# Performance work log

Measured on AMD Instinct MI355X. Metric: run time of the kernel, lower is better.

Reference implementation:

```python
import jax, jax.numpy as jnp
import numpy as np

B, S = 32, 128
VIDEO_SIZE, TITLE_SIZE = 768, 768
NUM_TAG, NUM_VOCAB, HIDDEN = 10000, 21128, 256


def setup_inputs() -> dict:
    key = jax.random.key(0)
    ks = jax.random.split(key, 10)
    video_feature = jax.random.normal(ks[0], (B, VIDEO_SIZE), dtype=jnp.float32)
    title_feature = jax.random.normal(ks[1], (B, S, TITLE_SIZE), dtype=jnp.float32)
    label_tag = jax.random.uniform(ks[2], (B, NUM_TAG), dtype=jnp.float32)
    label_mlm = jax.random.randint(ks[3], (B, S), 0, NUM_VOCAB, dtype=jnp.int64)
    Wt = jax.random.normal(ks[4], (NUM_TAG, VIDEO_SIZE), dtype=jnp.float32) * 0.02
    bt = jnp.zeros((NUM_TAG,), dtype=jnp.float32)
    Wm = jax.random.normal(ks[5], (NUM_VOCAB, TITLE_SIZE), dtype=jnp.float32) * 0.02
    bm = jnp.zeros((NUM_VOCAB,), dtype=jnp.float32)
    Wh = jax.random.normal(ks[6], (HIDDEN, VIDEO_SIZE + TITLE_SIZE), dtype=jnp.float32) * 0.02
    bh = jnp.zeros((HIDDEN,), dtype=jnp.float32)
    return {
        "video_feature": video_feature,
        "title_feature": title_feature,
        "label_tag": label_tag,
        "label_mlm": label_mlm,
        "Wt": Wt, "bt": bt, "Wm": Wm, "bm": bm, "Wh": Wh, "bh": bh,
    }


def reference(video_feature, title_feature, label_tag, label_mlm, Wt, bt, Wm, bm, Wh, bh):
    # tag head + BCEWithLogits (mean reduction), numerically stable form
    pred_tag = video_feature @ Wt.T + bt                       # [B, NUM_TAG]
    loss_tag = jnp.mean(
        jnp.maximum(pred_tag, 0.0) - pred_tag * label_tag
        + jnp.log1p(jnp.exp(-jnp.abs(pred_tag)))
    )
    pred_tag_sig = jax.nn.sigmoid(pred_tag)

    # mlm head: per-token vocab logits, masked CE summed over nonzero labels
    logits = jnp.einsum('bsd,vd->bsv', title_feature, Wm) + bm  # [B, S, V]
    lse = jax.nn.logsumexp(logits, axis=-1)                     # [B, S]
    gold = jnp.take_along_axis(logits, label_mlm[..., None], axis=-1)[..., 0]
    ce = lse - gold                                             # per-token NLL
    mask = (label_mlm != 0)
    loss_mlm = jnp.sum(jnp.where(mask, ce, 0.0))

    # fused embedding head + L2 normalize (torch eps 1e-12)
    feature = jnp.concatenate([video_feature, title_feature[:, 0]], axis=1)
    embedding = feature @ Wh.T + bh                             # [B, HIDDEN]
    norm = jnp.linalg.norm(embedding, axis=1, keepdims=True)
    normed_embedding = embedding / jnp.maximum(norm, 1e-12)

    return (pred_tag_sig, normed_embedding, loss_tag, loss_mlm)
```

## Files before the change

### kernel.cpp

```cpp
#include <hip/hip_runtime.h>
#include <hip/hip_bf16.h>
#include <math.h>

typedef short bf16x8 __attribute__((ext_vector_type(8)));
typedef float f32x4 __attribute__((ext_vector_type(4)));
typedef long i64x2 __attribute__((ext_vector_type(2)));

#define KDIM 768
#define NTAG 10000
#define NVOC 21128
#define HID 256
#define NTOK 4096
#define NCHUNK 24
#define CHUNK 881
#define NTILE 56
#define M0 4.0f
#define WMSCALE 16.0f
#define INVSCALE 0.0625f
#define LOG2E 1.44269504f

#define WS_A     0ull
#define WS_AVID  3145728ull
#define WS_PSUM  3194880ull
#define WS_GOLD  3588096ull
#define WS_TAGL  3604480ull
#define WS_WM8   3604544ull
#define WS_NEED  (WS_WM8 + 16226304ull + 65536ull)

#define OUT_EMB  320000
#define OUT_LTAG 328192
#define OUT_LMLM 328193

#define TAG_BLKS 313
#define GOLD_BLKS 1024
#define EMB_BLKS 32

typedef const __attribute__((address_space(1))) unsigned int glds_g;
typedef __attribute__((address_space(3))) unsigned int glds_l;

static __device__ __forceinline__ unsigned short f2bf(float f) {
  unsigned u = __builtin_bit_cast(unsigned, f);
  u = u + 0x7FFFu + ((u >> 16) & 1u);
  return (unsigned short)(u >> 16);
}

static __device__ __forceinline__ int pk4_fp8(float4 v, float scale) {
  int w = __builtin_amdgcn_cvt_pk_fp8_f32(v.x * scale, v.y * scale, 0, false);
  w = __builtin_amdgcn_cvt_pk_fp8_f32(v.z * scale, v.w * scale, w, true);
  return w;
}

__global__ __launch_bounds__(256) void k_conv(
    const float* __restrict__ title, const float* __restrict__ video,
    const float* __restrict__ Wm,
    char* __restrict__ A8, unsigned short* __restrict__ Avid,
    char* __restrict__ Wm8, float* __restrict__ tagSum) {
  const int nT = 393216;
  const int nV = 3072;
  const int nW = 2028288;
  int i = blockIdx.x * 256 + threadIdx.x;
  if (i == 0) tagSum[0] = 0.f;
  if (i < nT) {
    float4 v0 = ((const float4*)title)[i * 2];
    float4 v1 = ((const float4*)title)[i * 2 + 1];
    int2 o = {pk4_fp8(v0, 1.f), pk4_fp8(v1, 1.f)};
    *(int2*)(A8 + (size_t)i * 8) = o;
  } else if (i < nT + nV) {
    int j = i - nT;
    float4 v0 = ((const float4*)video)[j * 2];
    float4 v1 = ((const float4*)video)[j * 2 + 1];
    bf16x8 o;
    o[0] = (short)f2bf(v0.x); o[1] = (short)f2bf(v0.y);
    o[2] = (short)f2bf(v0.z); o[3] = (short)f2bf(v0.w);
    o[4] = (short)f2bf(v1.x); o[5] = (short)f2bf(v1.y);
    o[6] = (short)f2bf(v1.z); o[7] = (short)f2bf(v1.w);
    *(bf16x8*)(Avid + (size_t)j * 8) = o;
  } else {
    int j = i - nT - nV;
    if (j >= nW) return;
    float4 v0 = ((const float4*)Wm)[j * 2];
    float4 v1 = ((const float4*)Wm)[j * 2 + 1];
    int2 o = {pk4_fp8(v0, WMSCALE), pk4_fp8(v1, WMSCALE)};
    int row = j / 96;
    int koff = (j % 96) * 8;
    int kk2 = koff >> 6, w = koff & 63;
    int h = w >> 5, gg = (w & 31) >> 3;
    *(int2*)(Wm8 + (size_t)row * KDIM + kk2 * 64 + gg * 16 + h * 8) = o;
  }
}

template<bool WM8>
__global__ __launch_bounds__(256)
__attribute__((amdgpu_waves_per_eu(3, 3)))
void k_mlm(
    const char* __restrict__ A8,
    const float* __restrict__ Wm,
    const char* __restrict__ Wm8,
    const float* __restrict__ bm,
    float* __restrict__ psum) {
  __shared__ __align__(1024) char Bsm[4][12288];
  __shared__ float biasS[NTILE * 16];
  const int tid = threadIdx.x;
  const int lane = tid & 63, g = lane >> 4, col = lane & 15;
  const int wave = tid >> 6;
  const int chunk = blockIdx.x % NCHUNK, mt = blockIdx.x / NCHUNK;
  const int nbeg = chunk * CHUNK;
  const int nend = min(nbeg + CHUNK, NVOC);

  for (int i = tid; i < NTILE * 16; i += 256) {
    int n = nbeg + i;
    biasS[i] = (n < nend) ? (bm[n] - M0) * LOG2E : -1e30f;
  }

  const int arow0 = mt * 128 + wave * 32;
  long a0[24], a1[24];
  #pragma unroll
  for (int kk = 0; kk < 24; ++kk) {
    a0[kk] = *(const long*)(A8 + (size_t)(arow0 + col) * KDIM + kk * 32 + g * 8);
    a1[kk] = *(const long*)(A8 + (size_t)(arow0 + 16 + col) * KDIM + kk * 32 + g * 8);
  }

  float s[8];
  #pragma unroll
  for (int i = 0; i < 8; ++i) s[i] = 0.f;

  int e[3];
  #pragma unroll
  for (int j = 0; j < 3; ++j) {
    int sg = j * 256 + tid;
    e[j] = (sg & 15) * KDIM + (sg >> 6) * 64 + ((sg >> 4) & 3) * 16;
  }

  const int off0 = col * 16 + g * 256;
  const float kinv = INVSCALE * LOG2E;

  auto COMPUTE = [&](int t) {
    const char* B = &Bsm[t & 3][0] + off0;
    f32x4 acc0 = {0.f, 0.f, 0.f, 0.f}, acc1 = {0.f, 0.f, 0.f, 0.f};
    #pragma unroll
    for (int kk2 = 0; kk2 < 12; ++kk2) {
      i64x2 b = *(const i64x2*)(B + kk2 * 1024);
      acc0 = __builtin_amdgcn_mfma_f32_16x16x32_fp8_fp8(a0[2 * kk2], b[0], acc0, 0, 0, 0);
      acc1 = __builtin_amdgcn_mfma_f32_16x16x32_fp8_fp8(a1[2 * kk2], b[0], acc1, 0, 0, 0);
      acc0 = __builtin_amdgcn_mfma_f32_16x16x32_fp8_fp8(a0[2 * kk2 + 1], b[1], acc0, 0, 0, 0);
      acc1 = __builtin_amdgcn_mfma_f32_16x16x32_fp8_fp8(a1[2 * kk2 + 1], b[1], acc1, 0, 0, 0);
    }
    const float bias2 = biasS[t * 16 + col];
    #pragma unroll
    for (int rr = 0; rr < 4; ++rr) {
      s[rr]     += exp2f(fmaf(acc0[rr], kinv, bias2));
      s[rr + 4] += exp2f(fmaf(acc1[rr], kinv, bias2));
    }
  };

  if constexpr (WM8) {
    auto STAGE = [&](int buf, int tt) {
      const char* src = Wm8 + (size_t)(nbeg + tt * 16) * KDIM;
      char* dst = &Bsm[buf][0] + wave * 1024;
      #pragma unroll
      for (int j = 0; j < 3; ++j) {
        __builtin_amdgcn_global_load_lds((glds_g*)(src + e[j]),
                                         (glds_l*)(dst + j * 4096), 16, 0, 0);
      }
    };
    STAGE(0, 0); STAGE(1, 1); STAGE(2, 2);
    asm volatile("s_waitcnt lgkmcnt(0)" ::: "memory");
    for (int t = 0; t < NTILE; ++t) {
      asm volatile("s_waitcnt vmcnt(6)" ::: "memory");
      __builtin_amdgcn_s_barrier();
      __builtin_amdgcn_sched_barrier(0);
      int tp = t + 3;
      STAGE((t + 3) & 3, (tp < NTILE) ? tp : 0);
      __builtin_amdgcn_s_setprio(1);
      COMPUTE(t);
      __builtin_amdgcn_s_setprio(0);
      __builtin_amdgcn_sched_barrier(0);
    }
  } else {
    __syncthreads();
    for (int t = 0; t < NTILE; ++t) {
      #pragma unroll
      for (int j = 0; j < 3; ++j) {
        int sg = j * 256 + tid;
        int n = nbeg + t * 16 + (sg & 15);
        int kk2 = sg >> 6, gg = (sg >> 4) & 3;
        int4 o = {0, 0, 0, 0};
        if (n < NVOC) {
          const float* wp = Wm + (size_t)n * KDIM + kk2 * 64 + gg * 8;
          float4 f0 = ((const float4*)wp)[0], f1 = ((const float4*)wp)[1];
          float4 f2 = ((const float4*)(wp + 32))[0], f3 = ((const float4*)(wp + 32))[1];
          o.x = pk4_fp8(f0, WMSCALE); o.y = pk4_fp8(f1, WMSCALE);
          o.z = pk4_fp8(f2, WMSCALE); o.w = pk4_fp8(f3, WMSCALE);
        }
        *(int4*)(&Bsm[0][0] + sg * 16) = o;
      }
      __syncthreads();
      COMPUTE(t);
      __syncthreads();
    }
  }

  #pragma unroll
  for (int i = 0; i < 8; ++i) {
    float v = s[i];
    v += __shfl_xor(v, 1);
    v += __shfl_xor(v, 2);
    v += __shfl_xor(v, 4);
    v += __shfl_xor(v, 8);
    s[i] = v;
  }
  if (col == 0) {
    #pragma unroll
    for (int mblk = 0; mblk < 2; ++mblk)
      #pragma unroll
      for (int rr = 0; rr < 4; ++rr) {
        int tok = arow0 + mblk * 16 + g * 4 + rr;
        psum[tok * NCHUNK + chunk] = s[mblk * 4 + rr];
      }
  }
}

__global__ __launch_bounds__(256) void k_tail(
    const unsigned short* __restrict__ Avid,
    const float* __restrict__ Wt, const float* __restrict__ bt,
    const float* __restrict__ ylab,
    const float* __restrict__ title, const int* __restrict__ lab,
    const float* __restrict__ Wm, const float* __restrict__ bm,
    const float* __restrict__ video,
    const float* __restrict__ Wh, const float* __restrict__ bh,
    float* __restrict__ out_sig, float* __restrict__ tagSum,
    float* __restrict__ gold, float* __restrict__ out_emb) {
  __shared__ __align__(1024) char smem[49664];
  const int bid = blockIdx.x, tid = threadIdx.x;
  const int wave = tid >> 6, lane = tid & 63, g = lane >> 4, col = lane & 15;

  if (bid < TAG_BLKS) {
    unsigned short* Bt = (unsigned short*)smem;
    float* wsum = (float*)(smem + 49152);
    #pragma unroll
    for (int j = 0; j < 12; ++j) {
      int sg = j * 256 + tid;
      int tt = (j >= 6) ? 1 : 0;
      int sgl = sg - tt * 1536;
      int kk = sgl >> 6, c = (sgl & 63) >> 2, gg = sgl & 3;
      int n = (bid * 2 + tt) * 16 + c;
      bf16x8 o = {};
      if (n < NTAG) {
        const float* wp = Wt + (size_t)n * KDIM + kk * 32 + gg * 8;
        float4 f0 = ((const float4*)wp)[0], f1 = ((const float4*)wp)[1];
        o[0] = (short)f2bf(f0.x); o[1] = (short)f2bf(f0.y);
        o[2] = (short)f2bf(f0.z); o[3] = (short)f2bf(f0.w);
        o[4] = (short)f2bf(f1.x); o[5] = (short)f2bf(f1.y);
        o[6] = (short)f2bf(f1.z); o[7] = (short)f2bf(f1.w);
      }
      *(bf16x8*)((char*)Bt + sg * 16) = o;
    }
    __syncthreads();

    const int ntile = bid * 2 + (wave >> 1), mhalf = wave & 1;
    float lacc = 0.f;
    if (ntile < 625) {
      bf16x8 a[24];
      #pragma unroll
      for (int kk = 0; kk < 24; ++kk)
        a[kk] = *(const bf16x8*)(Avid + (size_t)(mhalf * 16 + col) * KDIM + kk * 32 + g * 8);
      const char* Bb = (const char*)Bt + (wave >> 1) * 24576 + col * 64 + g * 16;
      f32x4 acc = {0.f, 0.f, 0.f, 0.f};
      #pragma unroll
      for (int kk = 0; kk < 24; ++kk) {
        bf16x8 b = *(const bf16x8*)(Bb + kk * 1024);
        acc = __builtin_amdgcn_mfma_f32_16x16x32_bf16(a[kk], b, acc, 0, 0, 0);
      }
      const int nc = ntile * 16 + col;
      if (nc < NTAG) {
        const float bias = bt[nc];
        #pragma unroll
        for (int rr = 0; rr < 4; ++rr) {
          int brow = mhalf * 16 + g * 4 + rr;
          float x = acc[rr] + bias;
          out_sig[(size_t)brow * NTAG + nc] = 1.f / (1.f + __expf(-x));
          float y = ylab[(size_t)brow * NTAG + nc];
          lacc += fmaxf(x, 0.f) - x * y + log1pf(__expf(-fabsf(x)));
        }
      }
    }
    #pragma unroll
    for (int m = 32; m; m >>= 1) lacc += __shfl_xor(lacc, m);
    if (lane == 0) wsum[wave] = lacc;
    __syncthreads();
    if (tid == 0) atomicAdd(tagSum, wsum[0] + wsum[1] + wsum[2] + wsum[3]);

  } else if (bid < TAG_BLKS + GOLD_BLKS) {
    int tok = (bid - TAG_BLKS) * 4 + wave;
    int l = lab[tok];
    float acc = 0.f;
    #pragma unroll
    for (int j = 0; j < 12; ++j) {
      int k = j * 64 + lane;
      acc += title[(size_t)tok * KDIM + k] * Wm[(size_t)l * KDIM + k];
    }
    #pragma unroll
    for (int m = 32; m; m >>= 1) acc += __shfl_xor(acc, m);
    if (lane == 0) gold[tok] = acc + bm[l];

  } else {
    float* feat = (float*)smem;
    float* red = (float*)(smem + 49152);
    const int b = bid - TAG_BLKS - GOLD_BLKS;
    #pragma unroll
    for (int j = 0; j < 6; ++j) {
      int k = j * 256 + tid;
      feat[k] = (k < KDIM) ? video[(size_t)b * KDIM + k]
                           : title[(size_t)b * 128 * KDIM + (k - KDIM)];
    }
    __syncthreads();
    float acc = bh[tid];
    #pragma unroll 8
    for (int k = 0; k < 1536; k += 4) {
      float4 w = *(const float4*)(Wh + (size_t)tid * 1536 + k);
      acc += w.x * feat[k] + w.y * feat[k + 1] + w.z * feat[k + 2] + w.w * feat[k + 3];
    }
    float ss = acc * acc;
    #pragma unroll
    for (int m = 32; m; m >>= 1) ss += __shfl_xor(ss, m);
    if (lane == 0) red[wave] = ss;
    __syncthreads();
    float nrm = sqrtf(red[0] + red[1] + red[2] + red[3]);
    float scale = 1.f / fmaxf(nrm, 1e-12f);
    out_emb[(size_t)b * HID + tid] = acc * scale;
  }
}

__global__ __launch_bounds__(256) void k_final(
    const float* __restrict__ psum, const float* __restrict__ gold,
    const int* __restrict__ lab, const float* __restrict__ tagSum,
    float* __restrict__ out) {
  __shared__ float red[4];
  const int tid = threadIdx.x, wave = tid >> 6, lane = tid & 63;
  if (tid == 0) out[OUT_LTAG] = tagSum[0] / 320000.f;

  float lm = 0.f;
  for (int tok = tid; tok < NTOK; tok += 256) {
    float S = 0.f;
    #pragma unroll
    for (int c = 0; c < NCHUNK; ++c) S += psum[tok * NCHUNK + c];
    float lse = M0 + logf(S);
    if (lab[tok] != 0) lm += lse - gold[tok];
  }
  #pragma unroll
  for (int m = 32; m; m >>= 1) lm += __shfl_xor(lm, m);
  if (lane == 0) red[wave] = lm;
  __syncthreads();
  if (tid == 0) out[OUT_LMLM] = red[0] + red[1] + red[2] + red[3];
}

extern "C" void kernel_launch(void* const* d_in, const int* in_sizes, int n_in,
                              void* d_out, int out_size, void* d_ws, size_t ws_size,
                              hipStream_t stream) {
  const float* video = (const float*)d_in[0];
  const float* title = (const float*)d_in[1];
  const float* ylab  = (const float*)d_in[2];
  const int*   lab   = (const int*)d_in[3];
  const float* Wt = (const float*)d_in[4];
  const float* bt = (const float*)d_in[5];
  const float* Wm = (const float*)d_in[6];
  const float* bm = (const float*)d_in[7];
  const float* Wh = (const float*)d_in[8];
  const float* bh = (const float*)d_in[9];
  float* out = (float*)d_out;
  char* ws = (char*)d_ws;

  char* wsA8   = ws + WS_A;
  unsigned short* wsAvid = (unsigned short*)(ws + WS_AVID);
  float* wsPsum = (float*)(ws + WS_PSUM);
  float* wsGold = (float*)(ws + WS_GOLD);
  float* wsTagl = (float*)(ws + WS_TAGL);
  char* wsWm8  = ws + WS_WM8;

  const bool useWm8 = ws_size >= WS_NEED;

  k_conv<<<9471, 256, 0, stream>>>(title, video, Wm, wsA8, wsAvid, wsWm8, wsTagl);
  if (useWm8)
    k_mlm<true><<<768, 256, 0, stream>>>(wsA8, Wm, wsWm8, bm, wsPsum);
  else
    k_mlm<false><<<768, 256, 0, stream>>>(wsA8, Wm, wsWm8, bm, wsPsum);
  k_tail<<<TAG_BLKS + GOLD_BLKS + EMB_BLKS, 256, 0, stream>>>(
      wsAvid, Wt, bt, ylab, title, lab, Wm, bm, video, Wh, bh,
      out, wsTagl, wsGold, out + OUT_EMB);
  k_final<<<1, 256, 0, stream>>>(wsPsum, wsGold, lab, wsTagl, out);
}
```

Before: 196.1 us.

## Use plain row-major fp8 Wm with XOR-swizzled LDS and double buffering

```diff
diff --git a/kernel.cpp b/kernel.cpp
--- a/kernel.cpp
+++ b/kernel.cpp
@@ -4,7 +4,6 @@
 
 typedef short bf16x8 __attribute__((ext_vector_type(8)));
 typedef float f32x4 __attribute__((ext_vector_type(4)));
-typedef long i64x2 __attribute__((ext_vector_type(2)));
 
 #define KDIM 768
 #define NTAG 10000
@@ -81,11 +80,7 @@
     float4 v0 = ((const float4*)Wm)[j * 2];
     float4 v1 = ((const float4*)Wm)[j * 2 + 1];
     int2 o = {pk4_fp8(v0, WMSCALE), pk4_fp8(v1, WMSCALE)};
-    int row = j / 96;
-    int koff = (j % 96) * 8;
-    int kk2 = koff >> 6, w = koff & 63;
-    int h = w >> 5, gg = (w & 31) >> 3;
-    *(int2*)(Wm8 + (size_t)row * KDIM + kk2 * 64 + gg * 16 + h * 8) = o;
+    *(int2*)(Wm8 + (size_t)j * 8) = o;
   }
 }
 
@@ -98,7 +93,7 @@
     const char* __restrict__ Wm8,
     const float* __restrict__ bm,
     float* __restrict__ psum) {
-  __shared__ __align__(1024) char Bsm[4][12288];
+  __shared__ __align__(1024) char Bsm[2][12288];
   __shared__ float biasS[NTILE * 16];
   const int tid = threadIdx.x;
   const int lane = tid & 63, g = lane >> 4, col = lane & 15;
@@ -128,22 +123,24 @@
   #pragma unroll
   for (int j = 0; j < 3; ++j) {
     int sg = j * 256 + tid;
-    e[j] = (sg & 15) * KDIM + (sg >> 6) * 64 + ((sg >> 4) & 3) * 16;
-  }
-
-  const int off0 = col * 16 + g * 256;
+    int kk2 = sg >> 6, nl = (sg >> 2) & 15, q = sg & 3;
+    int qp = q ^ ((nl >> 1) & 3);
+    e[j] = nl * KDIM + kk2 * 64 + qp * 16;
+  }
+
+  const int off0 = col * 64 + ((g * 8) ^ (((col >> 1) & 3) << 4));
   const float kinv = INVSCALE * LOG2E;
 
   auto COMPUTE = [&](int t) {
-    const char* B = &Bsm[t & 3][0] + off0;
+    const char* Bb = &Bsm[t & 1][0];
+    const char* B0 = Bb + off0;
+    const char* B1 = Bb + (off0 ^ 32);
     f32x4 acc0 = {0.f, 0.f, 0.f, 0.f}, acc1 = {0.f, 0.f, 0.f, 0.f};
     #pragma unroll
-    for (int kk2 = 0; kk2 < 12; ++kk2) {
-      i64x2 b = *(const i64x2*)(B + kk2 * 1024);
-      acc0 = __builtin_amdgcn_mfma_f32_16x16x32_fp8_fp8(a0[2 * kk2], b[0], acc0, 0, 0, 0);
-      acc1 = __builtin_amdgcn_mfma_f32_16x16x32_fp8_fp8(a1[2 * kk2], b[0], acc1, 0, 0, 0);
-      acc0 = __builtin_amdgcn_mfma_f32_16x16x32_fp8_fp8(a0[2 * kk2 + 1], b[1], acc0, 0, 0, 0);
-      acc1 = __builtin_amdgcn_mfma_f32_16x16x32_fp8_fp8(a1[2 * kk2 + 1], b[1], acc1, 0, 0, 0);
+    for (int kk = 0; kk < 24; ++kk) {
+      long b = *(const long*)(((kk & 1) ? B1 : B0) + (kk >> 1) * 1024);
+      acc0 = __builtin_amdgcn_mfma_f32_16x16x32_fp8_fp8(a0[kk], b, acc0, 0, 0, 0);
+      acc1 = __builtin_amdgcn_mfma_f32_16x16x32_fp8_fp8(a1[kk], b, acc1, 0, 0, 0);
     }
     const float bias2 = biasS[t * 16 + col];
     #pragma unroll
@@ -163,18 +160,20 @@
                                          (glds_l*)(dst + j * 4096), 16, 0, 0);
       }
     };
-    STAGE(0, 0); STAGE(1, 1); STAGE(2, 2);
+    STAGE(0, 0);
     asm volatile("s_waitcnt lgkmcnt(0)" ::: "memory");
+    __builtin_amdgcn_s_barrier();
     for (int t = 0; t < NTILE; ++t) {
-      asm volatile("s_waitcnt vmcnt(6)" ::: "memory");
+      int tn = (t + 1 < NTILE) ? t + 1 : 0;
+      STAGE((t + 1) & 1, tn);
+      asm volatile("s_waitcnt vmcnt(3)" ::: "memory");
       __builtin_amdgcn_s_barrier();
       __builtin_amdgcn_sched_barrier(0);
-      int tp = t + 3;
-      STAGE((t + 3) & 3, (tp < NTILE) ? tp : 0);
       __builtin_amdgcn_s_setprio(1);
       COMPUTE(t);
       __builtin_amdgcn_s_setprio(0);
       __builtin_amdgcn_sched_barrier(0);
+      __builtin_amdgcn_s_barrier();
     }
   } else {
     __syncthreads();
@@ -182,13 +181,15 @@
       #pragma unroll
       for (int j = 0; j < 3; ++j) {
         int sg = j * 256 + tid;
-        int n = nbeg + t * 16 + (sg & 15);
-        int kk2 = sg >> 6, gg = (sg >> 4) & 3;
+        int n = nbeg + t * 16 + ((sg >> 2) & 15);
+        int kk2 = sg >> 6, q = sg & 3;
+        int qp = q ^ ((((sg >> 2) & 15) >> 1) & 3);
+        int koff = kk2 * 64 + qp * 16;
         int4 o = {0, 0, 0, 0};
         if (n < NVOC) {
-          const float* wp = Wm + (size_t)n * KDIM + kk2 * 64 + gg * 8;
+          const float* wp = Wm + (size_t)n * KDIM + koff;
           float4 f0 = ((const float4*)wp)[0], f1 = ((const float4*)wp)[1];
-          float4 f2 = ((const float4*)(wp + 32))[0], f3 = ((const float4*)(wp + 32))[1];
+          float4 f2 = ((const float4*)wp)[2], f3 = ((const float4*)wp)[3];
           o.x = pk4_fp8(f0, WMSCALE); o.y = pk4_fp8(f1, WMSCALE);
           o.z = pk4_fp8(f2, WMSCALE); o.w = pk4_fp8(f3, WMSCALE);
         }
```

Result: faster. 188.1 us (-4.1%).
